# Optimization experiments

Measured on AMD Instinct MI355X. Metric: run time of the kernel, lower is better.

## Reference

```python
import jax, jax.numpy as jnp
import numpy as np

LN_EPS = 1e-5

def _layernorm(x, g, b):
    mu = jnp.mean(x, axis=-1, keepdims=True)
    var = jnp.mean(jnp.square(x - mu), axis=-1, keepdims=True)
    return (x - mu) * jax.lax.rsqrt(var + LN_EPS) * g + b

def setup_inputs() -> dict:
    key = jax.random.key(0)
    ks = jax.random.split(key, 12)
    N0, N1, D0, D1, DO, E = 50000, 50000, 256, 512, 256, 1600000
    return {
        "x0": jax.random.normal(ks[0], (N0, D0), jnp.float32),
        "x1": jax.random.normal(ks[1], (N1, D1), jnp.float32),
        "W0": jax.random.normal(ks[2], (D0, DO), jnp.float32) * 0.05,
        "W1": jax.random.normal(ks[3], (D1, DO), jnp.float32) * 0.05,
        "Wres1": jax.random.normal(ks[4], (D1, DO), jnp.float32) * 0.05,
        "g0": jnp.ones((DO,), jnp.float32),
        "b0": jnp.zeros((DO,), jnp.float32),
        "g1": jnp.ones((DO,), jnp.float32),
        "b1": jnp.zeros((DO,), jnp.float32),
        "ew0": jax.random.uniform(ks[5], (E,), jnp.float32),
        "ew1": jax.random.uniform(ks[6], (E,), jnp.float32),
        "row0": jax.random.randint(ks[7], (E,), 0, N0, jnp.int32),
        "col0": jax.random.randint(ks[8], (E,), 0, N0, jnp.int32),
        "row1": jax.random.randint(ks[9], (E,), 0, N1, jnp.int32),
        "col1": jax.random.randint(ks[10], (E,), 0, N1, jnp.int32),
    }

def _gcn_type(x, W, ew, row, col, g, b, res):
    # h_proj = x @ W ; h_agg[i] = sum_{e: row_e=i} ew_e * h_proj[col_e]  (== spmm(adj, h_proj))
    h_proj = x @ W
    msgs = ew[:, None] * h_proj[col]                      # [E, DO] gather + scale
    h_agg = jax.ops.segment_sum(msgs, row, num_segments=x.shape[0])
    return _layernorm(h_agg + res, g, b)

def reference(x0, x1, W0, W1, Wres1, g0, b0, g1, b1, ew0, ew1, row0, col0, row1, col1):
    out0 = _gcn_type(x0, W0, ew0, row0, col0, g0, b0, x0)          # identity residual
    out1 = _gcn_type(x1, W1, ew1, row1, col1, g1, b1, x1 @ Wres1)  # projected residual
    return jnp.concatenate([out0, out1], axis=0)
```

## Files before the change

kernel.cpp:

```cpp
#include <hip/hip_runtime.h>
#include <hip/hip_bf16.h>
#include <cstddef>

typedef unsigned short u16;
typedef u16 u16x8 __attribute__((ext_vector_type(8)));
typedef __bf16 bf16x8 __attribute__((ext_vector_type(8)));
typedef float f32x4 __attribute__((ext_vector_type(4)));
typedef int i32x4 __attribute__((ext_vector_type(4)));
typedef float f32x4v __attribute__((ext_vector_type(4)));

__device__ __forceinline__ u16 f2b(float f) {
  unsigned int u = __float_as_uint(f);
  unsigned int r = 0x7FFFu + ((u >> 16) & 1u);
  return (u16)((u + r) >> 16);
}
__device__ __forceinline__ float b2f(u16 u) {
  return __uint_as_float(((unsigned int)u) << 16);
}

template <bool OUT_BF16>
__global__ __launch_bounds__(256) void gemm_bf16(
    const float* __restrict__ A, const u16* __restrict__ Bt, void* __restrict__ Cv,
    int M, int K) {
  __shared__ u16 As[64 * 64];
  __shared__ u16 Bs[256 * 64];
  const int tid = threadIdx.x;
  const int wid = tid >> 6;
  const int lane = tid & 63;
  const int brow = blockIdx.x * 64;
  const int waveN = wid * 64;
  const int q = lane >> 4;
  const int rl = lane & 15;

  f32x4 acc[4][4] = {};

  const int arow = tid >> 2;
  const int kq = (tid & 3) * 16;
  const int garow = brow + arow;
  const bool aok = garow < M;
  const int aswz = arow & 7;
  const int brb = tid;
  const int bswz = brb & 7;

  for (int k0 = 0; k0 < K; k0 += 64) {
    {
      const float* src = A + (size_t)garow * K + k0 + kq;
      u16* dstrow = As + arow * 64;
#pragma unroll
      for (int j = 0; j < 2; ++j) {
        float4 v0 = make_float4(0.f, 0.f, 0.f, 0.f), v1 = v0;
        if (aok) {
          v0 = *(const float4*)(src + j * 8);
          v1 = *(const float4*)(src + j * 8 + 4);
        }
        u16x8 v = {f2b(v0.x), f2b(v0.y), f2b(v0.z), f2b(v0.w),
                   f2b(v1.x), f2b(v1.y), f2b(v1.z), f2b(v1.w)};
        const int c = (kq >> 3) + j;
        *(u16x8*)(dstrow + 8 * (c ^ aswz)) = v;
      }
    }
    {
      const u16* src = Bt + (size_t)brb * K + k0;
      u16* dstrow = Bs + brb * 64;
#pragma unroll
      for (int j = 0; j < 8; ++j) {
        u16x8 v = *(const u16x8*)(src + j * 8);
        *(u16x8*)(dstrow + 8 * (j ^ bswz)) = v;
      }
    }
    __syncthreads();
#pragma unroll
    for (int ks = 0; ks < 2; ++ks) {
      bf16x8 af[4], bfr[4];
      const int cbase = ks * 4 + q;
#pragma unroll
      for (int i = 0; i < 4; ++i) {
        const int r = 16 * i + rl;
        af[i] = __builtin_bit_cast(bf16x8,
                 *(const u16x8*)(As + r * 64 + 8 * (cbase ^ (rl & 7))));
      }
#pragma unroll
      for (int j = 0; j < 4; ++j) {
        const int r = waveN + 16 * j + rl;
        bfr[j] = __builtin_bit_cast(bf16x8,
                  *(const u16x8*)(Bs + r * 64 + 8 * (cbase ^ (rl & 7))));
      }
#pragma unroll
      for (int i = 0; i < 4; ++i)
#pragma unroll
        for (int j = 0; j < 4; ++j)
          acc[i][j] = __builtin_amdgcn_mfma_f32_16x16x32_bf16(af[i], bfr[j], acc[i][j], 0, 0, 0);
    }
    __syncthreads();
  }

#pragma unroll
  for (int i = 0; i < 4; ++i) {
#pragma unroll
    for (int reg = 0; reg < 4; ++reg) {
      const int gr = brow + 16 * i + q * 4 + reg;
      if (gr >= M) continue;
#pragma unroll
      for (int j = 0; j < 4; ++j) {
        const int col = waveN + 16 * j + rl;
        const float v = acc[i][j][reg];
        if (OUT_BF16) ((u16*)Cv)[(size_t)gr * 256 + col] = f2b(v);
        else          ((float*)Cv)[(size_t)gr * 256 + col] = v;
      }
    }
  }
}

__global__ __launch_bounds__(256) void conv_wt(const float* __restrict__ W,
                                               u16* __restrict__ Wt, int K) {
  const int idx = blockIdx.x * 256 + threadIdx.x;
  const int k = idx >> 8;
  const int n = idx & 255;
  if (k < K) Wt[(size_t)n * K + k] = f2b(W[idx]);
}

#define EB   256
#define RPB  128
#define NBUK 391

__device__ __forceinline__ void edge_range(int E, int blk, int& s, int& e) {
  const int per = (((E + EB - 1) / EB) + 3) & ~3;
  s = blk * per;
  e = min(E, s + per);
}

__global__ __launch_bounds__(256) void pa_hist(const int* __restrict__ row,
                                               int* __restrict__ ghist, int E) {
  __shared__ int h[NBUK];
  for (int i = threadIdx.x; i < NBUK; i += 256) h[i] = 0;
  __syncthreads();
  int s, e;
  edge_range(E, blockIdx.x, s, e);
  for (int i = s + threadIdx.x * 4; i < e; i += 1024) {
    if (i + 3 < e) {
      const i32x4 rr = __builtin_nontemporal_load((const i32x4*)(row + i));
#pragma unroll
      for (int j = 0; j < 4; ++j) atomicAdd(&h[rr[j] >> 7], 1);
    } else {
      for (int i2 = i; i2 < e; ++i2) atomicAdd(&h[row[i2] >> 7], 1);
    }
  }
  __syncthreads();
  for (int i = threadIdx.x; i < NBUK; i += 256) ghist[i * EB + blockIdx.x] = h[i];
}

__global__ __launch_bounds__(256) void pa_scatter(
    const int* __restrict__ row, const int* __restrict__ col, const float* __restrict__ ew,
    const int* __restrict__ gscan, int2* __restrict__ tmp, int E) {
  __shared__ int cur[NBUK];
  for (int i = threadIdx.x; i < NBUK; i += 256) cur[i] = gscan[i * EB + blockIdx.x];
  __syncthreads();
  int s, e;
  edge_range(E, blockIdx.x, s, e);
  for (int i0 = s + threadIdx.x * 4; i0 < e; i0 += 1024) {
    if (i0 + 3 < e) {
      const i32x4 r4 = __builtin_nontemporal_load((const i32x4*)(row + i0));
      const i32x4 c4 = __builtin_nontemporal_load((const i32x4*)(col + i0));
      const f32x4 w4 = __builtin_nontemporal_load((const f32x4*)(ew + i0));
#pragma unroll
      for (int j = 0; j < 4; ++j) {
        const int pos = atomicAdd(&cur[r4[j] >> 7], 1);
        tmp[pos] = make_int2(((r4[j] & 127) << 16) | c4[j], __float_as_int(w4[j]));
      }
    } else {
      for (int i2 = i0; i2 < e; ++i2) {
        const int r = row[i2];
        const int pos = atomicAdd(&cur[r >> 7], 1);
        tmp[pos] = make_int2(((r & 127) << 16) | col[i2], __float_as_int(ew[i2]));
      }
    }
  }
}

__global__ __launch_bounds__(256) void pb_sort(
    const int2* __restrict__ tmp, const int* __restrict__ gscan,
    int2* __restrict__ sedge, int* __restrict__ offs, int E, int N) {
  __shared__ int h[RPB];
  __shared__ int sc[RPB];
  __shared__ int cur[RPB];
  const int b = blockIdx.x;
  const int t = threadIdx.x;
  const int base = gscan[b * EB];
  const int end = (b == NBUK - 1) ? E : gscan[(b + 1) * EB];
  if (t < RPB) h[t] = 0;
  __syncthreads();
  for (int i = base + t; i < end; i += 256) atomicAdd(&h[(tmp[i].x >> 16) & 127], 1);
  __syncthreads();
  if (t < RPB) sc[t] = h[t];
  __syncthreads();
  for (int off = 1; off < RPB; off <<= 1) {
    int x = (t >= off && t < RPB) ? sc[t - off] : 0;
    __syncthreads();
    if (t < RPB) sc[t] += x;
    __syncthreads();
  }
  if (t < RPB) {
    const int ex = base + sc[t] - h[t];
    cur[t] = ex;
    const int rg = b * RPB + t;
    if (rg <= N) offs[rg] = ex;
  }
  __syncthreads();
  for (int i = base + t; i < end; i += 256) {
    const int2 v = tmp[i];
    const int pos = atomicAdd(&cur[(v.x >> 16) & 127], 1);
    sedge[pos] = make_int2(v.x & 0xFFFF, v.y);
  }
}

__global__ __launch_bounds__(256) void scan1(const int* __restrict__ deg,
                                             int* __restrict__ offs,
                                             int* __restrict__ partials, int n) {
  __shared__ int sh[256];
  const int t = threadIdx.x;
  const int base = blockIdx.x * 1024 + t * 4;
  int v[4];
#pragma unroll
  for (int j = 0; j < 4; j++) v[j] = (base + j < n) ? deg[base + j] : 0;
  const int tsum = v[0] + v[1] + v[2] + v[3];
  sh[t] = tsum;
  __syncthreads();
  for (int off = 1; off < 256; off <<= 1) {
    int x = (t >= off) ? sh[t - off] : 0;
    __syncthreads();
    sh[t] += x;
    __syncthreads();
  }
  if (t == 255) partials[blockIdx.x] = sh[255];
  int run = sh[t] - tsum;
#pragma unroll
  for (int j = 0; j < 4; j++) {
    if (base + j < n) offs[base + j] = run;
    run += v[j];
  }
}

__global__ void scan2(int* __restrict__ partials, int nb) {
  if (threadIdx.x == 0 && blockIdx.x == 0) {
    int run = 0;
    for (int i = 0; i < nb; i++) {
      int t = partials[i];
      partials[i] = run;
      run += t;
    }
  }
}

__global__ __launch_bounds__(256) void scan_add(int* __restrict__ a,
                                                const int* __restrict__ partials, int n) {
  const int t = threadIdx.x;
  const int base = blockIdx.x * 1024 + t * 4;
  const int add = partials[blockIdx.x];
#pragma unroll
  for (int j = 0; j < 4; j++)
    if (base + j < n) a[base + j] += add;
}

__global__ __launch_bounds__(256) void agg_ln(
    const u16* __restrict__ hpb, const int* __restrict__ offs,
    const int2* __restrict__ sedge,
    const float* __restrict__ res, const float* __restrict__ g, const float* __restrict__ b,
    float* __restrict__ out, int nrows) {
  const int wave = threadIdx.x >> 6;
  const int lane = threadIdx.x & 63;
  const int r = blockIdx.x * 4 + wave;
  if (r >= nrows) return;
  const int half = lane >> 5;
  const int f8 = (lane & 31) * 8;
  const long long* sedge8 = (const long long*)sedge;

  float acc8[8] = {0.f, 0.f, 0.f, 0.f, 0.f, 0.f, 0.f, 0.f};
  int k = offs[r];
  const int kend = offs[r + 1];

  for (; k + 15 < kend; k += 16) {
    long long e[8];
#pragma unroll
    for (int j = 0; j < 8; ++j)
      e[j] = __builtin_nontemporal_load(sedge8 + k + half + 2 * j);
    u16x8 h[8];
#pragma unroll
    for (int j = 0; j < 8; ++j)
      h[j] = *(const u16x8*)(hpb + (size_t)(int)(e[j] & 0xFFFFFFFFll) * 256 + f8);
#pragma unroll
    for (int j = 0; j < 8; ++j) {
      const float w = __int_as_float((int)(e[j] >> 32));
#pragma unroll
      for (int d = 0; d < 8; ++d) acc8[d] += w * b2f(h[j][d]);
    }
  }
  for (; k + 7 < kend; k += 8) {
    long long e[4];
#pragma unroll
    for (int j = 0; j < 4; ++j)
      e[j] = __builtin_nontemporal_load(sedge8 + k + half + 2 * j);
    u16x8 h[4];
#pragma unroll
    for (int j = 0; j < 4; ++j)
      h[j] = *(const u16x8*)(hpb + (size_t)(int)(e[j] & 0xFFFFFFFFll) * 256 + f8);
#pragma unroll
    for (int j = 0; j < 4; ++j) {
      const float w = __int_as_float((int)(e[j] >> 32));
#pragma unroll
      for (int d = 0; d < 8; ++d) acc8[d] += w * b2f(h[j][d]);
    }
  }
  for (int kc = k + half; kc < kend; kc += 2) {
    const long long e = sedge8[kc];
    const float w = __int_as_float((int)(e >> 32));
    const u16x8 h = *(const u16x8*)(hpb + (size_t)(int)(e & 0xFFFFFFFFll) * 256 + f8);
#pragma unroll
    for (int d = 0; d < 8; ++d) acc8[d] += w * b2f(h[d]);
  }

#pragma unroll
  for (int d = 0; d < 8; ++d) acc8[d] += __shfl_xor(acc8[d], 32);

  {
    const f32x4 r0 = __builtin_nontemporal_load((const f32x4*)(res + (size_t)r * 256 + f8));
    const f32x4 r1 = __builtin_nontemporal_load((const f32x4*)(res + (size_t)r * 256 + f8 + 4));
#pragma unroll
    for (int d = 0; d < 4; ++d) { acc8[d] += r0[d]; acc8[4 + d] += r1[d]; }
  }

  float s = 0.f;
#pragma unroll
  for (int d = 0; d < 8; ++d) s += acc8[d];
#pragma unroll
  for (int m = 32; m >= 1; m >>= 1) s += __shfl_xor(s, m);
  const float mu = s * (1.f / 512.f);
#pragma unroll
  for (int d = 0; d < 8; ++d) acc8[d] -= mu;
  float ss = 0.f;
#pragma unroll
  for (int d = 0; d < 8; ++d) ss += acc8[d] * acc8[d];
#pragma unroll
  for (int m = 32; m >= 1; m >>= 1) ss += __shfl_xor(ss, m);
  const float rs = rsqrtf(ss * (1.f / 512.f) + 1e-5f);

  if (half == 0) {
    const float4 g0v = *(const float4*)(g + f8);
    const float4 g1v = *(const float4*)(g + f8 + 4);
    const float4 b0v = *(const float4*)(b + f8);
    const float4 b1v = *(const float4*)(b + f8 + 4);
    f32x4 o0, o1;
    o0[0] = acc8[0] * rs * g0v.x + b0v.x;
    o0[1] = acc8[1] * rs * g0v.y + b0v.y;
    o0[2] = acc8[2] * rs * g0v.z + b0v.z;
    o0[3] = acc8[3] * rs * g0v.w + b0v.w;
    o1[0] = acc8[4] * rs * g1v.x + b1v.x;
    o1[1] = acc8[5] * rs * g1v.y + b1v.y;
    o1[2] = acc8[6] * rs * g1v.z + b1v.z;
    o1[3] = acc8[7] * rs * g1v.w + b1v.w;
    __builtin_nontemporal_store(o0, (f32x4*)(out + (size_t)r * 256 + f8));
    __builtin_nontemporal_store(o1, (f32x4*)(out + (size_t)r * 256 + f8 + 4));
  }
}

extern "C" void kernel_launch(void* const* d_in, const int* in_sizes, int n_in,
                              void* d_out, int out_size, void* d_ws, size_t ws_size,
                              hipStream_t stream) {
  const float* x0    = (const float*)d_in[0];
  const float* x1    = (const float*)d_in[1];
  const float* W0    = (const float*)d_in[2];
  const float* W1    = (const float*)d_in[3];
  const float* Wres1 = (const float*)d_in[4];
  const float* g0    = (const float*)d_in[5];
  const float* b0    = (const float*)d_in[6];
  const float* g1    = (const float*)d_in[7];
  const float* b1    = (const float*)d_in[8];
  const float* ew0   = (const float*)d_in[9];
  const float* ew1   = (const float*)d_in[10];
  const int*   row0  = (const int*)d_in[11];
  const int*   col0  = (const int*)d_in[12];
  const int*   row1  = (const int*)d_in[13];
  const int*   col1  = (const int*)d_in[14];
  float* out = (float*)d_out;

  const int N = 50000, D0 = 256, D1 = 512, DO = 256, E = 1600000;

  char* w = (char*)d_ws;
  u16*   hpb   = (u16*)  (w);
  u16*   wtb   = (u16*)  (w + 25600000);
  int2*  sedge = (int2*) (w + 25862144);
  int*   offs  = (int*)  (w + 38662144);
  int*   ghist = (int*)  (w + 38862160);
  int*   parts = (int*)  (w + 39262560);
  int2*  tmp   = (int2*) (w);

  float* out0 = out;
  float* out1 = out + (size_t)N * DO;

  const dim3 blk(256);
  const dim3 gemm_grid((N + 63) / 64);
  const dim3 agg_grid((N + 3) / 4);
  const int NGH = NBUK * EB;
  const int NBS = (NGH + 1023) / 1024;

  auto build_csr = [&](const int* row, const int* col, const float* ew) {
    pa_hist<<<dim3(EB), blk, 0, stream>>>(row, ghist, E);
    scan1<<<dim3(NBS), blk, 0, stream>>>(ghist, ghist, parts, NGH);
    scan2<<<dim3(1), dim3(64), 0, stream>>>(parts, NBS);
    scan_add<<<dim3(NBS), blk, 0, stream>>>(ghist, parts, NGH);
    pa_scatter<<<dim3(EB), blk, 0, stream>>>(row, col, ew, ghist, tmp, E);
    pb_sort<<<dim3(NBUK), blk, 0, stream>>>(tmp, ghist, sedge, offs, E, N);
  };

  build_csr(row0, col0, ew0);
  conv_wt<<<dim3(D0), blk, 0, stream>>>(W0, wtb, D0);
  gemm_bf16<true><<<gemm_grid, blk, 0, stream>>>(x0, wtb, hpb, N, D0);
  agg_ln<<<agg_grid, blk, 0, stream>>>(hpb, offs, sedge, x0, g0, b0, out0, N);

  conv_wt<<<dim3(D1), blk, 0, stream>>>(Wres1, wtb, D1);
  gemm_bf16<false><<<gemm_grid, blk, 0, stream>>>(x1, wtb, out1, N, D1);
  build_csr(row1, col1, ew1);
  conv_wt<<<dim3(D1), blk, 0, stream>>>(W1, wtb, D1);
  gemm_bf16<true><<<gemm_grid, blk, 0, stream>>>(x1, wtb, hpb, N, D1);
  agg_ln<<<agg_grid, blk, 0, stream>>>(hpb, offs, sedge, out1, g1, b1, out1, N);
}
```

Before: 694.5 us.

## Split neighbor aggregation into feature slices and separate LayerNorm kernel

Replaces the fused aggregate+LayerNorm kernel with two kernels. The first runs a 2D grid where each block handles one 32-feature slice (8 slices) for 4 rows, so the concurrently gathered part of the projected bf16 features is about 3.2MB and is more likely to stay in cache. It adds the residual and writes pre-norm rows to the output buffer. A second kernel then applies LayerNorm row by row. The trade-off is reading the edge list 8 times, gathering 64-byte segments that may waste cache-line bandwidth, more shuffle reductions, and an extra write/read pass over the output.

```diff
diff --git a/kernel.cpp b/kernel.cpp
--- a/kernel.cpp
+++ b/kernel.cpp
@@ -7,7 +7,6 @@
 typedef __bf16 bf16x8 __attribute__((ext_vector_type(8)));
 typedef float f32x4 __attribute__((ext_vector_type(4)));
 typedef int i32x4 __attribute__((ext_vector_type(4)));
-typedef float f32x4v __attribute__((ext_vector_type(4)));
 
 __device__ __forceinline__ u16 f2b(float f) {
   unsigned int u = __float_as_uint(f);
@@ -261,105 +260,87 @@
     if (base + j < n) a[base + j] += add;
 }
 
-__global__ __launch_bounds__(256) void agg_ln(
+__global__ __launch_bounds__(256) void agg_slice(
     const u16* __restrict__ hpb, const int* __restrict__ offs,
-    const int2* __restrict__ sedge,
-    const float* __restrict__ res, const float* __restrict__ g, const float* __restrict__ b,
+    const int2* __restrict__ sedge, const float* __restrict__ res,
+    float* __restrict__ hag, int nrows) {
+  const int wave = threadIdx.x >> 6;
+  const int lane = threadIdx.x & 63;
+  const int r = blockIdx.y * 4 + wave;
+  if (r >= nrows) return;
+  const int s = blockIdx.x;
+  const int g = lane >> 2;
+  const int dbase = s * 32 + (lane & 3) * 8;
+  const long long* sedge8 = (const long long*)sedge;
+
+  float acc[8] = {0.f, 0.f, 0.f, 0.f, 0.f, 0.f, 0.f, 0.f};
+  const int kbeg = offs[r], kend = offs[r + 1];
+  for (int k = kbeg; k < kend; k += 32) {
+    const int e0 = k + g, e1 = k + 16 + g;
+    const bool k0 = e0 < kend, k1 = e1 < kend;
+    long long ed0 = 0, ed1 = 0;
+    if (k0) ed0 = __builtin_nontemporal_load(sedge8 + e0);
+    if (k1) ed1 = __builtin_nontemporal_load(sedge8 + e1);
+    u16x8 h0 = {}, h1 = {};
+    if (k0) h0 = *(const u16x8*)(hpb + (size_t)(int)ed0 * 256 + dbase);
+    if (k1) h1 = *(const u16x8*)(hpb + (size_t)(int)ed1 * 256 + dbase);
+    if (k0) {
+      const float w = __int_as_float((int)(ed0 >> 32));
+#pragma unroll
+      for (int d = 0; d < 8; ++d) acc[d] += w * b2f(h0[d]);
+    }
+    if (k1) {
+      const float w = __int_as_float((int)(ed1 >> 32));
+#pragma unroll
+      for (int d = 0; d < 8; ++d) acc[d] += w * b2f(h1[d]);
+    }
+  }
+
+#pragma unroll
+  for (int m = 4; m <= 32; m <<= 1)
+#pragma unroll
+    for (int d = 0; d < 8; ++d) acc[d] += __shfl_xor(acc[d], m);
+
+  if (lane < 8) {
+    float a4[4];
+    if (lane < 4) { a4[0] = acc[0]; a4[1] = acc[1]; a4[2] = acc[2]; a4[3] = acc[3]; }
+    else          { a4[0] = acc[4]; a4[1] = acc[5]; a4[2] = acc[6]; a4[3] = acc[7]; }
+    const size_t off = (size_t)r * 256 + s * 32 + (lane & 3) * 8 + (lane >> 2) * 4;
+    const f32x4 rv = __builtin_nontemporal_load((const f32x4*)(res + off));
+    f32x4 o;
+#pragma unroll
+    for (int d = 0; d < 4; ++d) o[d] = a4[d] + rv[d];
+    __builtin_nontemporal_store(o, (f32x4*)(hag + off));
+  }
+}
+
+__global__ __launch_bounds__(256) void ln_rows(
+    const float* __restrict__ hag, const float* __restrict__ g, const float* __restrict__ b,
     float* __restrict__ out, int nrows) {
   const int wave = threadIdx.x >> 6;
   const int lane = threadIdx.x & 63;
   const int r = blockIdx.x * 4 + wave;
   if (r >= nrows) return;
-  const int half = lane >> 5;
-  const int f8 = (lane & 31) * 8;
-  const long long* sedge8 = (const long long*)sedge;
-
-  float acc8[8] = {0.f, 0.f, 0.f, 0.f, 0.f, 0.f, 0.f, 0.f};
-  int k = offs[r];
-  const int kend = offs[r + 1];
-
-  for (; k + 15 < kend; k += 16) {
-    long long e[8];
-#pragma unroll
-    for (int j = 0; j < 8; ++j)
-      e[j] = __builtin_nontemporal_load(sedge8 + k + half + 2 * j);
-    u16x8 h[8];
-#pragma unroll
-    for (int j = 0; j < 8; ++j)
-      h[j] = *(const u16x8*)(hpb + (size_t)(int)(e[j] & 0xFFFFFFFFll) * 256 + f8);
-#pragma unroll
-    for (int j = 0; j < 8; ++j) {
-      const float w = __int_as_float((int)(e[j] >> 32));
-#pragma unroll
-      for (int d = 0; d < 8; ++d) acc8[d] += w * b2f(h[j][d]);
-    }
-  }
-  for (; k + 7 < kend; k += 8) {
-    long long e[4];
-#pragma unroll
-    for (int j = 0; j < 4; ++j)
-      e[j] = __builtin_nontemporal_load(sedge8 + k + half + 2 * j);
-    u16x8 h[4];
-#pragma unroll
-    for (int j = 0; j < 4; ++j)
-      h[j] = *(const u16x8*)(hpb + (size_t)(int)(e[j] & 0xFFFFFFFFll) * 256 + f8);
-#pragma unroll
-    for (int j = 0; j < 4; ++j) {
-      const float w = __int_as_float((int)(e[j] >> 32));
-#pragma unroll
-      for (int d = 0; d < 8; ++d) acc8[d] += w * b2f(h[j][d]);
-    }
-  }
-  for (int kc = k + half; kc < kend; kc += 2) {
-    const long long e = sedge8[kc];
-    const float w = __int_as_float((int)(e >> 32));
-    const u16x8 h = *(const u16x8*)(hpb + (size_t)(int)(e & 0xFFFFFFFFll) * 256 + f8);
-#pragma unroll
-    for (int d = 0; d < 8; ++d) acc8[d] += w * b2f(h[d]);
-  }
-
-#pragma unroll
-  for (int d = 0; d < 8; ++d) acc8[d] += __shfl_xor(acc8[d], 32);
-
-  {
-    const f32x4 r0 = __builtin_nontemporal_load((const f32x4*)(res + (size_t)r * 256 + f8));
-    const f32x4 r1 = __builtin_nontemporal_load((const f32x4*)(res + (size_t)r * 256 + f8 + 4));
-#pragma unroll
-    for (int d = 0; d < 4; ++d) { acc8[d] += r0[d]; acc8[4 + d] += r1[d]; }
-  }
-
-  float s = 0.f;
-#pragma unroll
-  for (int d = 0; d < 8; ++d) s += acc8[d];
+  const int f4 = lane * 4;
+  f32x4 v = __builtin_nontemporal_load((const f32x4*)(hag + (size_t)r * 256 + f4));
+  float s = v[0] + v[1] + v[2] + v[3];
 #pragma unroll
   for (int m = 32; m >= 1; m >>= 1) s += __shfl_xor(s, m);
-  const float mu = s * (1.f / 512.f);
-#pragma unroll
-  for (int d = 0; d < 8; ++d) acc8[d] -= mu;
-  float ss = 0.f;
-#pragma unroll
-  for (int d = 0; d < 8; ++d) ss += acc8[d] * acc8[d];
+  const float mu = s * (1.f / 256.f);
+#pragma unroll
+  for (int d = 0; d < 4; ++d) v[d] -= mu;
+  float ss = v[0] * v[0] + v[1] * v[1] + v[2] * v[2] + v[3] * v[3];
 #pragma unroll
   for (int m = 32; m >= 1; m >>= 1) ss += __shfl_xor(ss, m);
-  const float rs = rsqrtf(ss * (1.f / 512.f) + 1e-5f);
-
-  if (half == 0) {
-    const float4 g0v = *(const float4*)(g + f8);
-    const float4 g1v = *(const float4*)(g + f8 + 4);
-    const float4 b0v = *(const float4*)(b + f8);
-    const float4 b1v = *(const float4*)(b + f8 + 4);
-    f32x4 o0, o1;
-    o0[0] = acc8[0] * rs * g0v.x + b0v.x;
-    o0[1] = acc8[1] * rs * g0v.y + b0v.y;
-    o0[2] = acc8[2] * rs * g0v.z + b0v.z;
-    o0[3] = acc8[3] * rs * g0v.w + b0v.w;
-    o1[0] = acc8[4] * rs * g1v.x + b1v.x;
-    o1[1] = acc8[5] * rs * g1v.y + b1v.y;
-    o1[2] = acc8[6] * rs * g1v.z + b1v.z;
-    o1[3] = acc8[7] * rs * g1v.w + b1v.w;
-    __builtin_nontemporal_store(o0, (f32x4*)(out + (size_t)r * 256 + f8));
-    __builtin_nontemporal_store(o1, (f32x4*)(out + (size_t)r * 256 + f8 + 4));
-  }
+  const float rs = rsqrtf(ss * (1.f / 256.f) + 1e-5f);
+  const float4 gg = *(const float4*)(g + f4);
+  const float4 bb = *(const float4*)(b + f4);
+  f32x4 o;
+  o[0] = v[0] * rs * gg.x + bb.x;
+  o[1] = v[1] * rs * gg.y + bb.y;
+  o[2] = v[2] * rs * gg.z + bb.z;
+  o[3] = v[3] * rs * gg.w + bb.w;
+  __builtin_nontemporal_store(o, (f32x4*)(out + (size_t)r * 256 + f4));
 }
 
 extern "C" void kernel_launch(void* const* d_in, const int* in_sizes, int n_in,
@@ -398,7 +379,8 @@
 
   const dim3 blk(256);
   const dim3 gemm_grid((N + 63) / 64);
-  const dim3 agg_grid((N + 3) / 4);
+  const dim3 slice_grid(8, (N + 3) / 4);
+  const dim3 ln_grid((N + 3) / 4);
   const int NGH = NBUK * EB;
   const int NBS = (NGH + 1023) / 1024;
 
@@ -414,12 +396,14 @@
   build_csr(row0, col0, ew0);
   conv_wt<<<dim3(D0), blk, 0, stream>>>(W0, wtb, D0);
   gemm_bf16<true><<<gemm_grid, blk, 0, stream>>>(x0, wtb, hpb, N, D0);
-  agg_ln<<<agg_grid, blk, 0, stream>>>(hpb, offs, sedge, x0, g0, b0, out0, N);
+  agg_slice<<<slice_grid, blk, 0, stream>>>(hpb, offs, sedge, x0, out0, N);
+  ln_rows<<<ln_grid, blk, 0, stream>>>(out0, g0, b0, out0, N);
 
   conv_wt<<<dim3(D1), blk, 0, stream>>>(Wres1, wtb, D1);
   gemm_bf16<false><<<gemm_grid, blk, 0, stream>>>(x1, wtb, out1, N, D1);
   build_csr(row1, col1, ew1);
   conv_wt<<<dim3(D1), blk, 0, stream>>>(W1, wtb, D1);
   gemm_bf16<true><<<gemm_grid, blk, 0, stream>>>(x1, wtb, hpb, N, D1);
-  agg_ln<<<agg_grid, blk, 0, stream>>>(hpb, offs, sedge, out1, g1, b1, out1, N);
-}
+  agg_slice<<<slice_grid, blk, 0, stream>>>(hpb, offs, sedge, out1, out1, N);
+  ln_rows<<<ln_grid, blk, 0, stream>>>(out1, g1, b1, out1, N);
+}
```

New measurement: 928.7 us. 1.34x slower.
